# Kernel optimization log

Hardware: AMD Instinct MI355X
Metric: run time of the kernel (lower is better)

The kernel has to match this reference:

```python
import jax, jax.numpy as jnp
import numpy as np


def setup_inputs() -> dict:
    key = jax.random.key(0)
    k1, k2 = jax.random.split(key)
    input = jax.random.normal(k1, (4, 2048, 2048), dtype=jnp.float32)
    target = jax.random.normal(k2, (4, 2048, 2048), dtype=jnp.float32) * 2.0 + 0.5
    return {"input": input, "target": target}


def _hist_match(source, template):
    """JAX histogram matching, equivalent to the numpy unique/cumsum/interp
    version for inputs with distinct values (true for continuous random data).

    For each source element x, its empirical quantile is
        q(x) = count(source <= x) / N  == s_quantiles[bin_idx] in the numpy code,
    computed via sort + searchsorted(side='right').
    The template CDF is the sorted template paired with quantiles (j+1)/M,
    matching cumsum(t_counts)/M at each (unique) value.
    """
    src = source.ravel()
    tmpl_sorted = jnp.sort(template.ravel())
    N = src.shape[0]
    M = tmpl_sorted.shape[0]
    s_sorted = jnp.sort(src)
    # rank of each element among all source elements (count <= x)
    ranks = jnp.searchsorted(s_sorted, src, side='right')
    s_q = ranks.astype(jnp.float32) / jnp.float32(N)
    t_q = jnp.arange(1, M + 1, dtype=jnp.float32) / jnp.float32(M)
    matched = jnp.interp(s_q, t_q, tmpl_sorted)
    return matched.reshape(source.shape)


def reference(input, target):
    # hist_match_torch.forward: matched histogram (non-differentiable in original)
    matched = jax.lax.stop_gradient(_hist_match(input, target))
    # HistogramLoss: (matched - input)^2 summed / numel
    loss = jnp.mean((matched - input) ** 2)
    # original forward returns `input`; the meaningful computed quantities are
    # the matched tensor and the loss, so we return both.
    return matched, loss
```

## Files before the change

### kernel.cpp

```cpp
#include <hip/hip_runtime.h>
#include <cstdint>


#define NBINS    8192u
#define HGX      512u
#define MGX      512u
#define KIN      2048u
#define KTG      4096u

__device__ __forceinline__ void bin_and_frac(float x, unsigned& b, float& frac) {
    float d = __builtin_fmaf(x, 256.0f, 4096.0f);
    d = fminf(fmaxf(d, 0.0f), 8191.999f);
    unsigned bb = (unsigned)d;
    b = bb;
    frac = d - (float)bb;
}

__global__ __launch_bounds__(512, 8) void hist_kernel(const float* __restrict__ in,
                                                      const float* __restrict__ tg,
                                                      unsigned* __restrict__ H, unsigned n16) {
    __shared__ unsigned h[NBINS];
    for (unsigned i = threadIdx.x; i < NBINS; i += 512) h[i] = 0;
    __syncthreads();
    const float* x = blockIdx.y ? tg : in;
    unsigned* Hh = H + blockIdx.y * NBINS;
    unsigned stride = gridDim.x * 512;
    for (unsigned i = blockIdx.x * 512 + threadIdx.x; i < n16; i += stride) {
        const float4* p = (const float4*)x + 4u * i;
        float4 a0 = p[0], a1 = p[1], a2 = p[2], a3 = p[3];
        float xs[16] = {a0.x, a0.y, a0.z, a0.w, a1.x, a1.y, a1.z, a1.w,
                        a2.x, a2.y, a2.z, a2.w, a3.x, a3.y, a3.z, a3.w};
        #pragma unroll
        for (int k = 0; k < 16; k++) {
            unsigned b; float f;
            bin_and_frac(xs[k], b, f);
            atomicAdd(&h[b], 1u);
        }
    }
    __syncthreads();
    for (unsigned i = threadIdx.x; i < NBINS; i += 512) {
        unsigned v = h[i];
        if (v) atomicAdd(&Hh[i], v);
    }
}

__global__ void scan_kernel(const unsigned* __restrict__ H, unsigned* __restrict__ C) {
    __shared__ unsigned s[1024];
    const unsigned* h = H + blockIdx.x * NBINS;
    unsigned* c = C + blockIdx.x * (NBINS + 1);
    unsigned base = threadIdx.x * 8;
    unsigned v[8]; unsigned own = 0;
    #pragma unroll
    for (int k = 0; k < 8; k++) { v[k] = h[base + k]; own += v[k]; }
    s[threadIdx.x] = own; __syncthreads();
    for (unsigned off = 1; off < 1024; off <<= 1) {
        unsigned t = (threadIdx.x >= off) ? s[threadIdx.x - off] : 0u;
        __syncthreads();
        s[threadIdx.x] += t;
        __syncthreads();
    }
    unsigned ex = s[threadIdx.x] - own;
    #pragma unroll
    for (int k = 0; k < 8; k++) { unsigned t = v[k]; c[base + k] = ex; ex += t; }
    if (threadIdx.x == 1023) c[NBINS] = s[1023];
}

__global__ void buildAB_kernel(const unsigned* __restrict__ Cin, const unsigned* __restrict__ Ctg,
                               float2* __restrict__ AB, int* __restrict__ hdr, unsigned n) {
    unsigned b = blockIdx.x * blockDim.x + threadIdx.x;
    if (b >= NBINS) return;
    unsigned r0 = Cin[b], r1 = Cin[b + 1];
    if (r1 <= KIN) atomicMax(&hdr[0], (int)b);
    if (r0 >= n - KIN) atomicMax(&hdr[1], (int)(8192u - b));
    unsigned t0 = Ctg[b], t1 = Ctg[b + 1];
    if (t1 <= KTG) atomicMax(&hdr[2], (int)b);
    if (t0 >= n - KTG) atomicMax(&hdr[3], (int)(8192u - b));
    if (r1 == r0) { AB[b] = make_float2(0.f, 0.f); return; }
    const float w = 32.0f / (float)NBINS;
    float v[2];
    unsigned rr[2] = {r0, r1};
    #pragma unroll
    for (int k = 0; k < 2; k++) {
        unsigned r = rr[k]; if (r > n - 1) r = n - 1;
        unsigned lo = 0, hi = NBINS;
        while (hi - lo > 1) { unsigned mid = (lo + hi) >> 1; if (Ctg[mid] <= r) lo = mid; else hi = mid; }
        unsigned c0 = Ctg[lo], c1 = Ctg[lo + 1];
        v[k] = -16.0f + (float)lo * w + w * ((float)(r - c0 + 1) / (float)(c1 - c0));
    }
    AB[b] = make_float2(v[0], v[1] - v[0]);
}

__global__ void exact_target_kernel(const float* __restrict__ tg_lo, const float* __restrict__ tg_hi,
                                    const unsigned* __restrict__ ctrs,
                                    float* __restrict__ Tlo, float* __restrict__ Thi) {
    __shared__ __align__(16) float v[KTG];
    int side = blockIdx.y;
    const float* src = side ? tg_hi : tg_lo;
    unsigned m = ctrs[side ? 3 : 2];
    if (m > KTG) m = KTG;
    float sgn = side ? -1.f : 1.f;
    for (unsigned k = threadIdx.x; k < m; k += 1024) v[k] = sgn * src[k];
    __syncthreads();
    unsigned j = blockIdx.x * 1024 + threadIdx.x;
    if (j >= m) return;
    float y = v[j];
    unsigned lt = 0, le = 0;
    unsigned m4 = m & ~3u;
    for (unsigned k = 0; k < m4; k += 4) {
        float4 z = *(const float4*)&v[k];
        lt += (z.x < y) + (z.y < y) + (z.z < y) + (z.w < y);
        le += (z.x <= y) + (z.y <= y) + (z.z <= y) + (z.w <= y);
    }
    for (unsigned k = m4; k < m; k++) { lt += (v[k] < y); le += (v[k] <= y); }
    float yo = sgn * y;
    if (side) {
        for (unsigned idx = KTG - le; idx < KTG - lt; idx++) Thi[idx] = yo;
    } else {
        for (unsigned r = lt; r < le; r++) Tlo[r] = yo;
    }
}

__global__ __launch_bounds__(512, 4) void matchcollect_kernel(
        const float* __restrict__ input, const float* __restrict__ target,
        const float2* __restrict__ AB, const int* __restrict__ hdr,
        float* __restrict__ vlo, unsigned* __restrict__ ilo,
        float* __restrict__ vhi, unsigned* __restrict__ ihi,
        float* __restrict__ tg_lo, float* __restrict__ tg_hi,
        unsigned* __restrict__ ctrs,
        float* __restrict__ out, float* __restrict__ bpart,
        unsigned n) {
    __shared__ float2 sAB[NBINS];
    unsigned n16 = n >> 4;
    unsigned stride = gridDim.x * 512;
    unsigned i0 = blockIdx.x * 512 + threadIdx.x;

    if (blockIdx.y == 1) {
        int blo = hdr[2], bhi = 8192 - hdr[3];
        for (unsigned i = i0; i < n16; i += stride) {
            const float4* p = (const float4*)target + 4u * i;
            float4 a0 = p[0], a1 = p[1], a2 = p[2], a3 = p[3];
            float xs[16] = {a0.x, a0.y, a0.z, a0.w, a1.x, a1.y, a1.z, a1.w,
                            a2.x, a2.y, a2.z, a2.w, a3.x, a3.y, a3.z, a3.w};
            unsigned b[16]; bool lo16[16], hi16[16]; bool any = false;
            #pragma unroll
            for (int k = 0; k < 16; k++) {
                float f;
                bin_and_frac(xs[k], b[k], f);
                lo16[k] = ((int)b[k] <= blo);
                hi16[k] = ((int)b[k] >= bhi);
                any = any || lo16[k] || hi16[k];
            }
            if (any) {
                #pragma unroll
                for (int k = 0; k < 16; k++) {
                    if (lo16[k]) { unsigned p2 = atomicAdd(&ctrs[2], 1u); tg_lo[p2] = xs[k]; }
                    else if (hi16[k]) { unsigned p2 = atomicAdd(&ctrs[3], 1u); tg_hi[p2] = xs[k]; }
                }
            }
        }
        return;
    }

    for (unsigned j = threadIdx.x; j < NBINS; j += 512) sAB[j] = AB[j];
    __syncthreads();

    int blo = hdr[0], bhi = 8192 - hdr[1];
    float acc = 0.f;
    for (unsigned i = i0; i < n16; i += stride) {
        const float4* p = (const float4*)input + 4u * i;
        float4 a0 = p[0], a1 = p[1], a2 = p[2], a3 = p[3];
        float xs[16] = {a0.x, a0.y, a0.z, a0.w, a1.x, a1.y, a1.z, a1.w,
                        a2.x, a2.y, a2.z, a2.w, a3.x, a3.y, a3.z, a3.w};
        unsigned b[16]; float fr[16];
        #pragma unroll
        for (int k = 0; k < 16; k++) bin_and_frac(xs[k], b[k], fr[k]);
        float2 ab[16];
        #pragma unroll
        for (int k = 0; k < 16; k++) ab[k] = sAB[b[k]];
        bool tl[16]; bool any = false;
        #pragma unroll
        for (int k = 0; k < 16; k++) {
            tl[k] = ((int)b[k] <= blo) || ((int)b[k] >= bhi);
            any = any || tl[k];
        }
        float m[16];
        #pragma unroll
        for (int k = 0; k < 16; k++) {
            m[k] = __builtin_fmaf(ab[k].y, fr[k], ab[k].x);
            float d = tl[k] ? 0.f : (m[k] - xs[k]);
            acc = __builtin_fmaf(d, d, acc);
        }
        float4* q = (float4*)out + 4u * i;
        q[0] = make_float4(m[0],  m[1],  m[2],  m[3]);
        q[1] = make_float4(m[4],  m[5],  m[6],  m[7]);
        q[2] = make_float4(m[8],  m[9],  m[10], m[11]);
        q[3] = make_float4(m[12], m[13], m[14], m[15]);
        if (any) {
            #pragma unroll
            for (int k = 0; k < 16; k++) {
                if (!tl[k]) continue;
                if ((int)b[k] <= blo) { unsigned p2 = atomicAdd(&ctrs[0], 1u); vlo[p2] = xs[k]; ilo[p2] = 16 * i + k; }
                else                  { unsigned p2 = atomicAdd(&ctrs[1], 1u); vhi[p2] = xs[k]; ihi[p2] = 16 * i + k; }
            }
        }
    }
    #pragma unroll
    for (int off = 32; off > 0; off >>= 1) acc += __shfl_down(acc, off, 64);
    if ((threadIdx.x & 63) == 0)
        bpart[blockIdx.x * 8 + (threadIdx.x >> 6)] = acc;
}

__global__ void loss_reduce_kernel(const float* __restrict__ bpart, float* __restrict__ loss,
                                   unsigned nb, unsigned n) {
    float s = 0.f;
    for (unsigned i = threadIdx.x; i < nb; i += 1024) s += bpart[i];
    #pragma unroll
    for (int off = 32; off > 0; off >>= 1) s += __shfl_down(s, off, 64);
    __shared__ float ws[16];
    int w = threadIdx.x >> 6;
    if ((threadIdx.x & 63) == 0) ws[w] = s;
    __syncthreads();
    if (threadIdx.x == 0) {
        float t = 0.f;
        #pragma unroll
        for (int k = 0; k < 16; k++) t += ws[k];
        *loss = t * (1.0f / (float)n);
    }
}

__global__ void exact_input_kernel(const float* __restrict__ in_lo_v, const unsigned* __restrict__ in_lo_i,
                                   const float* __restrict__ in_hi_v, const unsigned* __restrict__ in_hi_i,
                                   const unsigned* __restrict__ ctrs,
                                   const float* __restrict__ Tlo, const float* __restrict__ Thi,
                                   float* __restrict__ out, float* __restrict__ loss, unsigned n) {
    __shared__ __align__(16) float v[KIN];
    int side = blockIdx.y;
    const float* sv = side ? in_hi_v : in_lo_v;
    const unsigned* si = side ? in_hi_i : in_lo_i;
    unsigned m = ctrs[side ? 1 : 0];
    if (m > KIN) m = KIN;
    float sgn = side ? -1.f : 1.f;
    for (unsigned k = threadIdx.x; k < m; k += 1024) v[k] = sgn * sv[k];
    __syncthreads();
    unsigned j = blockIdx.x * 1024 + threadIdx.x;
    float d2 = 0.f;
    if (j < m) {
        float y = v[j];
        unsigned lt = 0, le = 0;
        unsigned m4 = m & ~3u;
        for (unsigned k = 0; k < m4; k += 4) {
            float4 z = *(const float4*)&v[k];
            lt += (z.x < y) + (z.y < y) + (z.z < y) + (z.w < y);
            le += (z.x <= y) + (z.y <= y) + (z.z <= y) + (z.w <= y);
        }
        for (unsigned k = m4; k < m; k++) { lt += (v[k] < y); le += (v[k] <= y); }
        float mv = side ? Thi[KTG - 1 - lt] : Tlo[le - 1];
        float x = sgn * y;
        out[si[j]] = mv;
        float d = mv - x;
        d2 = d * d;
    }
    #pragma unroll
    for (int off = 32; off > 0; off >>= 1) d2 += __shfl_down(d2, off, 64);
    if ((threadIdx.x & 63) == 0 && d2 != 0.f)
        atomicAdd(loss, d2 * (1.0f / (float)n));
}

extern "C" void kernel_launch(void* const* d_in, const int* in_sizes, int n_in,
                              void* d_out, int out_size, void* d_ws, size_t ws_size,
                              hipStream_t stream) {
    const float* input  = (const float*)d_in[0];
    const float* target = (const float*)d_in[1];
    unsigned n = (unsigned)in_sizes[0];
    float* out  = (float*)d_out;
    float* loss = out + n;

    char* wsb = (char*)d_ws;
    unsigned* H    = (unsigned*)(wsb);
    unsigned* Cin  = (unsigned*)(wsb + 64 * 1024);
    unsigned* Ctg  = Cin + (NBINS + 1);
    float2*   AB   = (float2*)  (wsb + 160 * 1024);
    char*     aux  = wsb + 224 * 1024;
    int*      hdr  = (int*)     (aux);
    unsigned* ctrs = (unsigned*)(aux + 16);
    float*    bpart= (float*)   (aux + 64);
    char*     tails= aux + 64 + 16384 + 64;
    float*    in_lo_v = (float*)   (tails);
    unsigned* in_lo_i = (unsigned*)(tails + KIN * 4);
    float*    in_hi_v = (float*)   (tails + KIN * 8);
    unsigned* in_hi_i = (unsigned*)(tails + KIN * 12);
    float*    tg_lo   = (float*)   (tails + KIN * 16);
    float*    tg_hi   = (float*)   (tails + KIN * 16 + KTG * 4);
    float*    Tlo     = (float*)   (tails + KIN * 16 + KTG * 8);
    float*    Thi     = (float*)   (tails + KIN * 16 + KTG * 12);

    (void)hipMemsetAsync(H, 0, 2 * NBINS * 4, stream);
    (void)hipMemsetAsync(hdr, 0, 32, stream);
    (void)hipMemsetAsync(loss, 0, 4, stream);

    unsigned n16 = n >> 4;

    hist_kernel<<<dim3(HGX, 2), 512, 0, stream>>>(input, target, H, n16);
    scan_kernel<<<2, 1024, 0, stream>>>(H, Cin);
    buildAB_kernel<<<NBINS / 256, 256, 0, stream>>>(Cin, Ctg, AB, hdr, n);

    matchcollect_kernel<<<dim3(MGX, 2), 512, 0, stream>>>(input, target, AB, hdr,
                                                          in_lo_v, in_lo_i, in_hi_v, in_hi_i,
                                                          tg_lo, tg_hi, ctrs, out, bpart, n);
    loss_reduce_kernel<<<1, 1024, 0, stream>>>(bpart, loss, MGX * 8, n);
    exact_target_kernel<<<dim3((KTG + 1023) / 1024, 2), 1024, 0, stream>>>(tg_lo, tg_hi, ctrs, Tlo, Thi);
    exact_input_kernel<<<dim3((KIN + 1023) / 1024, 2), 1024, 0, stream>>>(in_lo_v, in_lo_i, in_hi_v, in_hi_i,
                                                                          ctrs, Tlo, Thi, out, loss, n);
}
```

Measured before the change: 525.4 us.

## Use one-shot grid for match kernel with global AB lookups and nontemporal stores

The match/collect kernel drops its grid-stride loop and shared-memory AB table. It now launches one 256-thread block per chunk, gathers AB directly from global memory (L1/L2-cached) and writes the output with nontemporal stores. The histogram kernel processes 32 elements per thread per iteration. The goal is to remove the per-block 64KB LDS fill and raise occupancy and memory-level parallelism, at the cost of uncoalesced global gathers and a much larger partial-sum buffer that loss_reduce must sum.

```diff
diff --git a/kernel.cpp b/kernel.cpp
--- a/kernel.cpp
+++ b/kernel.cpp
@@ -4,9 +4,10 @@
 
 #define NBINS    8192u
 #define HGX      512u
-#define MGX      512u
 #define KIN      2048u
 #define KTG      4096u
+
+typedef float f32x4 __attribute__((ext_vector_type(4)));
 
 __device__ __forceinline__ void bin_and_frac(float x, unsigned& b, float& frac) {
     float d = __builtin_fmaf(x, 256.0f, 4096.0f);
@@ -16,22 +17,25 @@
     frac = d - (float)bb;
 }
 
-__global__ __launch_bounds__(512, 8) void hist_kernel(const float* __restrict__ in,
+__global__ __launch_bounds__(512, 4) void hist_kernel(const float* __restrict__ in,
                                                       const float* __restrict__ tg,
-                                                      unsigned* __restrict__ H, unsigned n16) {
+                                                      unsigned* __restrict__ H, unsigned n32) {
     __shared__ unsigned h[NBINS];
     for (unsigned i = threadIdx.x; i < NBINS; i += 512) h[i] = 0;
     __syncthreads();
     const float* x = blockIdx.y ? tg : in;
     unsigned* Hh = H + blockIdx.y * NBINS;
     unsigned stride = gridDim.x * 512;
-    for (unsigned i = blockIdx.x * 512 + threadIdx.x; i < n16; i += stride) {
-        const float4* p = (const float4*)x + 4u * i;
+    for (unsigned i = blockIdx.x * 512 + threadIdx.x; i < n32; i += stride) {
+        const float4* p = (const float4*)x + 8u * i;
         float4 a0 = p[0], a1 = p[1], a2 = p[2], a3 = p[3];
-        float xs[16] = {a0.x, a0.y, a0.z, a0.w, a1.x, a1.y, a1.z, a1.w,
-                        a2.x, a2.y, a2.z, a2.w, a3.x, a3.y, a3.z, a3.w};
-        #pragma unroll
-        for (int k = 0; k < 16; k++) {
+        float4 a4 = p[4], a5 = p[5], a6 = p[6], a7 = p[7];
+        float xs[32] = {a0.x, a0.y, a0.z, a0.w, a1.x, a1.y, a1.z, a1.w,
+                        a2.x, a2.y, a2.z, a2.w, a3.x, a3.y, a3.z, a3.w,
+                        a4.x, a4.y, a4.z, a4.w, a5.x, a5.y, a5.z, a5.w,
+                        a6.x, a6.y, a6.z, a6.w, a7.x, a7.y, a7.z, a7.w};
+        #pragma unroll
+        for (int k = 0; k < 32; k++) {
             unsigned b; float f;
             bin_and_frac(xs[k], b, f);
             atomicAdd(&h[b], 1u);
@@ -120,7 +124,7 @@
     }
 }
 
-__global__ __launch_bounds__(512, 4) void matchcollect_kernel(
+__global__ __launch_bounds__(256, 8) void matchcollect_kernel(
         const float* __restrict__ input, const float* __restrict__ target,
         const float2* __restrict__ AB, const int* __restrict__ hdr,
         float* __restrict__ vlo, unsigned* __restrict__ ilo,
@@ -129,14 +133,12 @@
         unsigned* __restrict__ ctrs,
         float* __restrict__ out, float* __restrict__ bpart,
         unsigned n) {
-    __shared__ float2 sAB[NBINS];
     unsigned n16 = n >> 4;
-    unsigned stride = gridDim.x * 512;
-    unsigned i0 = blockIdx.x * 512 + threadIdx.x;
+    unsigned i = blockIdx.x * 256 + threadIdx.x;
 
     if (blockIdx.y == 1) {
-        int blo = hdr[2], bhi = 8192 - hdr[3];
-        for (unsigned i = i0; i < n16; i += stride) {
+        if (i < n16) {
+            int blo = hdr[2], bhi = 8192 - hdr[3];
             const float4* p = (const float4*)target + 4u * i;
             float4 a0 = p[0], a1 = p[1], a2 = p[2], a3 = p[3];
             float xs[16] = {a0.x, a0.y, a0.z, a0.w, a1.x, a1.y, a1.z, a1.w,
@@ -161,12 +163,9 @@
         return;
     }
 
-    for (unsigned j = threadIdx.x; j < NBINS; j += 512) sAB[j] = AB[j];
-    __syncthreads();
-
-    int blo = hdr[0], bhi = 8192 - hdr[1];
     float acc = 0.f;
-    for (unsigned i = i0; i < n16; i += stride) {
+    if (i < n16) {
+        int blo = hdr[0], bhi = 8192 - hdr[1];
         const float4* p = (const float4*)input + 4u * i;
         float4 a0 = p[0], a1 = p[1], a2 = p[2], a3 = p[3];
         float xs[16] = {a0.x, a0.y, a0.z, a0.w, a1.x, a1.y, a1.z, a1.w,
@@ -174,27 +173,33 @@
         unsigned b[16]; float fr[16];
         #pragma unroll
         for (int k = 0; k < 16; k++) bin_and_frac(xs[k], b[k], fr[k]);
-        float2 ab[16];
-        #pragma unroll
-        for (int k = 0; k < 16; k++) ab[k] = sAB[b[k]];
+        float m[16];
+        #pragma unroll
+        for (int g = 0; g < 2; g++) {
+            float2 ab[8];
+            #pragma unroll
+            for (int k = 0; k < 8; k++) ab[k] = AB[b[8 * g + k]];
+            #pragma unroll
+            for (int k = 0; k < 8; k++)
+                m[8 * g + k] = __builtin_fmaf(ab[k].y, fr[8 * g + k], ab[k].x);
+        }
         bool tl[16]; bool any = false;
         #pragma unroll
         for (int k = 0; k < 16; k++) {
             tl[k] = ((int)b[k] <= blo) || ((int)b[k] >= bhi);
             any = any || tl[k];
-        }
-        float m[16];
-        #pragma unroll
-        for (int k = 0; k < 16; k++) {
-            m[k] = __builtin_fmaf(ab[k].y, fr[k], ab[k].x);
             float d = tl[k] ? 0.f : (m[k] - xs[k]);
             acc = __builtin_fmaf(d, d, acc);
         }
-        float4* q = (float4*)out + 4u * i;
-        q[0] = make_float4(m[0],  m[1],  m[2],  m[3]);
-        q[1] = make_float4(m[4],  m[5],  m[6],  m[7]);
-        q[2] = make_float4(m[8],  m[9],  m[10], m[11]);
-        q[3] = make_float4(m[12], m[13], m[14], m[15]);
+        f32x4* q = (f32x4*)out + 4u * i;
+        f32x4 o0 = {m[0],  m[1],  m[2],  m[3]};
+        f32x4 o1 = {m[4],  m[5],  m[6],  m[7]};
+        f32x4 o2 = {m[8],  m[9],  m[10], m[11]};
+        f32x4 o3 = {m[12], m[13], m[14], m[15]};
+        __builtin_nontemporal_store(o0, q + 0);
+        __builtin_nontemporal_store(o1, q + 1);
+        __builtin_nontemporal_store(o2, q + 2);
+        __builtin_nontemporal_store(o3, q + 3);
         if (any) {
             #pragma unroll
             for (int k = 0; k < 16; k++) {
@@ -207,7 +212,7 @@
     #pragma unroll
     for (int off = 32; off > 0; off >>= 1) acc += __shfl_down(acc, off, 64);
     if ((threadIdx.x & 63) == 0)
-        bpart[blockIdx.x * 8 + (threadIdx.x >> 6)] = acc;
+        bpart[blockIdx.x * 4 + (threadIdx.x >> 6)] = acc;
 }
 
 __global__ void loss_reduce_kernel(const float* __restrict__ bpart, float* __restrict__ loss,
@@ -284,7 +289,7 @@
     int*      hdr  = (int*)     (aux);
     unsigned* ctrs = (unsigned*)(aux + 16);
     float*    bpart= (float*)   (aux + 64);
-    char*     tails= aux + 64 + 16384 + 64;
+    char*     tails= aux + 64 + 65536 + 64;
     float*    in_lo_v = (float*)   (tails);
     unsigned* in_lo_i = (unsigned*)(tails + KIN * 4);
     float*    in_hi_v = (float*)   (tails + KIN * 8);
@@ -298,16 +303,18 @@
     (void)hipMemsetAsync(hdr, 0, 32, stream);
     (void)hipMemsetAsync(loss, 0, 4, stream);
 
+    unsigned n32 = n >> 5;
     unsigned n16 = n >> 4;
-
-    hist_kernel<<<dim3(HGX, 2), 512, 0, stream>>>(input, target, H, n16);
+    unsigned mgx = (n16 + 255) / 256;
+
+    hist_kernel<<<dim3(HGX, 2), 512, 0, stream>>>(input, target, H, n32);
     scan_kernel<<<2, 1024, 0, stream>>>(H, Cin);
     buildAB_kernel<<<NBINS / 256, 256, 0, stream>>>(Cin, Ctg, AB, hdr, n);
 
-    matchcollect_kernel<<<dim3(MGX, 2), 512, 0, stream>>>(input, target, AB, hdr,
+    matchcollect_kernel<<<dim3(mgx, 2), 256, 0, stream>>>(input, target, AB, hdr,
                                                           in_lo_v, in_lo_i, in_hi_v, in_hi_i,
                                                           tg_lo, tg_hi, ctrs, out, bpart, n);
-    loss_reduce_kernel<<<1, 1024, 0, stream>>>(bpart, loss, MGX * 8, n);
+    loss_reduce_kernel<<<1, 1024, 0, stream>>>(bpart, loss, mgx * 4, n);
     exact_target_kernel<<<dim3((KTG + 1023) / 1024, 2), 1024, 0, stream>>>(tg_lo, tg_hi, ctrs, Tlo, Thi);
     exact_input_kernel<<<dim3((KIN + 1023) / 1024, 2), 1024, 0, stream>>>(in_lo_v, in_lo_i, in_hi_v, in_hi_i,
                                                                           ctrs, Tlo, Thi, out, loss, n);
```

Measured after the change: 548.6 us. 4.4% more time.
